# Optimization experiments

Measured on AMD Instinct MI355X. Metric: run time of the kernel, lower is better.

Reference implementation:

```python
import jax, jax.numpy as jnp
import numpy as np

N, D_IN, D_OUT = 4096, 1024, 1024

def setup_inputs() -> dict:
    key = jax.random.key(0)
    k1, k2, k3, k4 = jax.random.split(key, 4)
    x = jax.random.normal(k1, (N, D_IN), dtype=jnp.float32)
    # original uses torch.rand (uniform [0,1)) for params
    w_query = jax.random.uniform(k2, (D_IN, D_OUT), dtype=jnp.float32)
    w_key = jax.random.uniform(k3, (D_IN, D_OUT), dtype=jnp.float32)
    w_value = jax.random.uniform(k4, (D_IN, D_OUT), dtype=jnp.float32)
    return {"x": x, "w_query": w_query, "w_key": w_key, "w_value": w_value}

def reference(x, w_query, w_key, w_value):
    queries = x @ w_query          # [N, d_out]
    keys = x @ w_key               # [N, d_out]
    values = x @ w_value           # [N, d_out]
    scale = keys.shape[-1] ** 0.5
    scores = queries @ keys.T      # [N, N]
    attn = jax.nn.softmax(scores / scale, axis=-1)
    return attn @ values           # [N, d_out]
```

## Files before the change

kernel.cpp:

```cpp
#include <hip/hip_runtime.h>
#include <math.h>

#define NROWS 4096
#define DDIM  1024

typedef __attribute__((ext_vector_type(8))) short short8;
typedef __attribute__((ext_vector_type(4))) float f32x4;

__device__ __forceinline__ ushort f2bf(float v) {
  union { float f; uint32_t u; } c; c.f = v;
  uint32_t u = c.u;
  uint32_t lsb = (u >> 16) & 1u;
  u += 0x7fffu + lsb;
  return (ushort)(u >> 16);
}
__device__ __forceinline__ float bf2f(ushort h) {
  union { uint32_t u; float f; } c; c.u = ((uint32_t)h) << 16;
  return c.f;
}

__device__ __forceinline__ size_t pidx(int r, int c, int ldt) {
  return ((size_t)((r >> 4) * ldt + (c >> 5))) * 512 +
         ((c >> 3) & 3) * 128 + (r & 15) * 8 + (c & 7);
}

__global__ __launch_bounds__(256) void prep(const float* __restrict__ x,
                                            const float* __restrict__ wq,
                                            const float* __restrict__ wk,
                                            const float* __restrict__ wv,
                                            ushort* Xh, ushort* Xl,
                                            ushort* Wqh, ushort* Wql,
                                            ushort* Wkh, ushort* Wkl, ushort* Wvh) {
  __shared__ float tl[32][33];
  const int b = blockIdx.x, t = threadIdx.x;
  if (b < 1024) {
    const float4* src = (const float4*)x;
#pragma unroll
    for (int r = 0; r < 4; ++r) {
      int i = b * 1024 + r * 256 + t;
      int row = i >> 8;
      int c = (i & 255) << 2;
      float4 v = src[i];
      ushort4 h, l;
      h.x = f2bf(v.x); l.x = f2bf(v.x - bf2f(h.x));
      h.y = f2bf(v.y); l.y = f2bf(v.y - bf2f(h.y));
      h.z = f2bf(v.z); l.z = f2bf(v.z - bf2f(h.z));
      h.w = f2bf(v.w); l.w = f2bf(v.w - bf2f(h.w));
      size_t o = pidx(row, c, DDIM / 32);
      *(ushort4*)(Xh + o) = h;
      *(ushort4*)(Xl + o) = l;
    }
  } else {
    const int z = (b - 1024) >> 10;
    const int tile = (b - 1024) & 1023;
    const float* src = z == 0 ? wq : (z == 1 ? wk : wv);
    ushort* dh = z == 0 ? Wqh : (z == 1 ? Wkh : Wvh);
    ushort* dl = z == 0 ? Wql : (z == 1 ? Wkl : nullptr);
    const int r0 = (tile >> 5) * 32;
    const int c0 = (tile & 31) * 32;
    const int tx = t & 31, ty = t >> 5;
    for (int i = ty; i < 32; i += 8)
      tl[i][tx] = src[(size_t)(r0 + i) * DDIM + c0 + tx];
    __syncthreads();
    for (int i = ty; i < 32; i += 8) {
      float v = tl[tx][i];
      ushort h = f2bf(v);
      size_t o = pidx(c0 + i, r0 + tx, DDIM / 32);
      dh[o] = h;
      if (dl) dl[o] = f2bf(v - bf2f(h));
    }
  }
}

template <bool SPLIT, int KT>
__device__ __forceinline__ void direct_gemm(const ushort* __restrict__ Ah,
                                            const ushort* __restrict__ Al,
                                            const ushort* __restrict__ Bh,
                                            const ushort* __restrict__ Bl,
                                            int m0, int n0, f32x4 (*acc)[4]) {
  const int t = threadIdx.x;
  const int wv = t >> 6, ln = t & 63;
  const int arb = (wv >> 1) * 64, crb = (wv & 1) * 64;
  const int ra = (m0 + arb) >> 4;
  const int rb = (n0 + crb) >> 4;
  const size_t ts = (size_t)KT * 512;

  size_t baseA[4], baseB[4];
#pragma unroll
  for (int i = 0; i < 4; ++i) baseA[i] = (size_t)(ra + i) * ts + ln * 8;
#pragma unroll
  for (int j = 0; j < 4; ++j) baseB[j] = (size_t)(rb + j) * ts + ln * 8;

#pragma unroll 2
  for (int s = 0; s < KT; ++s) {
    short8 ah[4], al[4];
#pragma unroll
    for (int i = 0; i < 4; ++i) {
      size_t o = baseA[i] + (size_t)s * 512;
      ah[i] = *(const short8*)(Ah + o);
      if constexpr (SPLIT) al[i] = *(const short8*)(Al + o);
    }
#pragma unroll
    for (int j = 0; j < 4; ++j) {
      size_t o = baseB[j] + (size_t)s * 512;
      short8 bh = *(const short8*)(Bh + o);
#pragma unroll
      for (int i = 0; i < 4; ++i)
        acc[i][j] = __builtin_amdgcn_mfma_f32_16x16x32_bf16(ah[i], bh, acc[i][j], 0, 0, 0);
      if constexpr (SPLIT) {
        short8 bl = *(const short8*)(Bl + o);
#pragma unroll
        for (int i = 0; i < 4; ++i) {
          acc[i][j] = __builtin_amdgcn_mfma_f32_16x16x32_bf16(ah[i], bl, acc[i][j], 0, 0, 0);
          acc[i][j] = __builtin_amdgcn_mfma_f32_16x16x32_bf16(al[i], bh, acc[i][j], 0, 0, 0);
        }
      }
    }
  }
}

__global__ __launch_bounds__(256) void gemm_qkv(const ushort* __restrict__ Xh,
                                                const ushort* __restrict__ Xl,
                                                const ushort* __restrict__ Wqh, const ushort* __restrict__ Wql,
                                                const ushort* __restrict__ Wkh, const ushort* __restrict__ Wkl,
                                                const ushort* __restrict__ Wvh,
                                                ushort* Qh, ushort* Ql, ushort* Kh, ushort* Kl, ushort* Vt) {
  const int which = blockIdx.x % 3;
  const int g = blockIdx.x / 3;
  const int by = blockIdx.y;
  const int t = threadIdx.x;
  const int wv = t >> 6, ln = t & 63;
  const int quad = ln >> 4, l16 = ln & 15;

  f32x4 acc[4][4];
#pragma unroll
  for (int i = 0; i < 4; ++i)
#pragma unroll
    for (int j = 0; j < 4; ++j) acc[i][j] = (f32x4){0.f, 0.f, 0.f, 0.f};

  if (which == 2) {
    const int m0 = g * 128;
    const int n0 = by * 128;
    direct_gemm<false, DDIM / 32>(Wvh, nullptr, Xh, nullptr, m0, n0, acc);
#pragma unroll
    for (int i = 0; i < 4; ++i)
#pragma unroll
      for (int j = 0; j < 4; ++j) {
        int kv = n0 + (wv & 1) * 64 + j * 16 + l16;
        int d = m0 + (wv >> 1) * 64 + i * 16 + quad * 4;
#pragma unroll
        for (int r2 = 0; r2 < 4; ++r2)
          Vt[pidx(d + r2, kv, NROWS / 32)] = f2bf(acc[i][j][r2]);
      }
  } else {
    const int n0 = g * 128;
    const int m0 = by * 128;
    const ushort* Bh = which ? Wkh : Wqh;
    const ushort* Bl = which ? Wkl : Wql;
    direct_gemm<true, DDIM / 32>(Xh, Xl, Bh, Bl, m0, n0, acc);
    const float scale = which ? 1.0f : 0.03125f;
    ushort* H = which ? Kh : Qh;
    ushort* L = which ? Kl : Ql;
#pragma unroll
    for (int i = 0; i < 4; ++i)
#pragma unroll
      for (int j = 0; j < 4; ++j) {
        int col = n0 + (wv & 1) * 64 + j * 16 + l16;
        int rw = m0 + (wv >> 1) * 64 + i * 16 + quad * 4;
#pragma unroll
        for (int r2 = 0; r2 < 4; ++r2) {
          float v = acc[i][j][r2] * scale;
          ushort h = f2bf(v);
          size_t o = pidx(rw + r2, col, DDIM / 32);
          H[o] = h;
          L[o] = f2bf(v - bf2f(h));
        }
      }
  }
}

__global__ __launch_bounds__(256) void gemm_s(const ushort* __restrict__ Qh, const ushort* __restrict__ Ql,
                                              const ushort* __restrict__ Kh, const ushort* __restrict__ Kl,
                                              float* __restrict__ S) {
  const int n0 = blockIdx.x * 128, m0 = blockIdx.y * 128;
  const int t = threadIdx.x;
  const int wv = t >> 6, ln = t & 63;
  const int quad = ln >> 4, l16 = ln & 15;

  f32x4 acc[4][4];
#pragma unroll
  for (int i = 0; i < 4; ++i)
#pragma unroll
    for (int j = 0; j < 4; ++j) acc[i][j] = (f32x4){0.f, 0.f, 0.f, 0.f};

  direct_gemm<true, DDIM / 32>(Qh, Ql, Kh, Kl, m0, n0, acc);

#pragma unroll
  for (int i = 0; i < 4; ++i)
#pragma unroll
    for (int j = 0; j < 4; ++j) {
      int col = n0 + (wv & 1) * 64 + j * 16 + l16;
      int rw = m0 + (wv >> 1) * 64 + i * 16 + quad * 4;
#pragma unroll
      for (int r2 = 0; r2 < 4; ++r2)
        S[(size_t)(rw + r2) * NROWS + col] = acc[i][j][r2];
    }
}

__global__ __launch_bounds__(256) void softmax_pack(const float* __restrict__ S,
                                                    ushort* __restrict__ P) {
  const int row = blockIdx.x, t = threadIdx.x;
  const float* Sr = S + (size_t)row * NROWS;
  const float4* S4 = (const float4*)Sr;
  float4 v[4];
  float mx = -3.4e38f;
#pragma unroll
  for (int c = 0; c < 4; ++c) {
    v[c] = S4[c * 256 + t];
    mx = fmaxf(mx, fmaxf(fmaxf(v[c].x, v[c].y), fmaxf(v[c].z, v[c].w)));
  }
  __shared__ float red[4];
  for (int o = 32; o >= 1; o >>= 1) mx = fmaxf(mx, __shfl_xor(mx, o));
  int wv = t >> 6, ln = t & 63;
  if (ln == 0) red[wv] = mx;
  __syncthreads();
  mx = fmaxf(fmaxf(red[0], red[1]), fmaxf(red[2], red[3]));
  float s = 0.f;
#pragma unroll
  for (int c = 0; c < 4; ++c) {
    v[c].x = __expf(v[c].x - mx);
    v[c].y = __expf(v[c].y - mx);
    v[c].z = __expf(v[c].z - mx);
    v[c].w = __expf(v[c].w - mx);
    s += v[c].x + v[c].y + v[c].z + v[c].w;
  }
  for (int o = 32; o >= 1; o >>= 1) s += __shfl_xor(s, o);
  __syncthreads();
  if (ln == 0) red[wv] = s;
  __syncthreads();
  s = red[0] + red[1] + red[2] + red[3];
  float inv = 1.f / s;
#pragma unroll
  for (int c = 0; c < 4; ++c) {
    ushort4 h;
    h.x = f2bf(v[c].x * inv);
    h.y = f2bf(v[c].y * inv);
    h.z = f2bf(v[c].z * inv);
    h.w = f2bf(v[c].w * inv);
    int c0 = 1024 * c + 4 * t;
    *(ushort4*)(P + pidx(row, c0, NROWS / 32)) = h;
  }
}

__global__ __launch_bounds__(256) void gemm_pv(const ushort* __restrict__ P,
                                               const ushort* __restrict__ Vt,
                                               float* __restrict__ Out) {
  const int n0 = blockIdx.x * 128, m0 = blockIdx.y * 128;
  const int t = threadIdx.x;
  const int wv = t >> 6, ln = t & 63;
  const int quad = ln >> 4, l16 = ln & 15;

  f32x4 acc[4][4];
#pragma unroll
  for (int i = 0; i < 4; ++i)
#pragma unroll
    for (int j = 0; j < 4; ++j) acc[i][j] = (f32x4){0.f, 0.f, 0.f, 0.f};

  direct_gemm<false, NROWS / 32>(P, nullptr, Vt, nullptr, m0, n0, acc);

#pragma unroll
  for (int i = 0; i < 4; ++i)
#pragma unroll
    for (int j = 0; j < 4; ++j) {
      int col = n0 + (wv & 1) * 64 + j * 16 + l16;
      int rw = m0 + (wv >> 1) * 64 + i * 16 + quad * 4;
#pragma unroll
      for (int r2 = 0; r2 < 4; ++r2)
        Out[(size_t)(rw + r2) * DDIM + col] = acc[i][j][r2];
    }
}

extern "C" void kernel_launch(void* const* d_in, const int* in_sizes, int n_in,
                              void* d_out, int out_size, void* d_ws, size_t ws_size,
                              hipStream_t stream) {
  const float* x  = (const float*)d_in[0];
  const float* wq = (const float*)d_in[1];
  const float* wk = (const float*)d_in[2];
  const float* wv = (const float*)d_in[3];
  char* ws = (char*)d_ws;
  const size_t MB = 1u << 20;

  ushort* Vt  = (ushort*)(ws + 0);
  ushort* Qh  = (ushort*)(ws + 8 * MB);
  ushort* Ql  = (ushort*)(ws + 16 * MB);
  ushort* Kh  = (ushort*)(ws + 24 * MB);
  ushort* Kl  = (ushort*)(ws + 32 * MB);
  ushort* Pp  = (ushort*)(ws + 8 * MB);
  ushort* Xh  = (ushort*)(ws + 40 * MB);
  ushort* Xl  = (ushort*)(ws + 48 * MB);
  ushort* Wqh = (ushort*)(ws + 56 * MB);
  ushort* Wql = (ushort*)(ws + 58 * MB);
  ushort* Wkh = (ushort*)(ws + 60 * MB);
  ushort* Wkl = (ushort*)(ws + 62 * MB);
  ushort* Wvh = (ushort*)(ws + 64 * MB);
  float*  S   = (float*)(ws + 40 * MB);
  float*  Out = (float*)d_out;

  prep<<<4096, 256, 0, stream>>>(x, wq, wk, wv, Xh, Xl, Wqh, Wql, Wkh, Wkl, Wvh);
  gemm_qkv<<<dim3(24, 32), 256, 0, stream>>>(Xh, Xl, Wqh, Wql, Wkh, Wkl, Wvh,
                                             Qh, Ql, Kh, Kl, Vt);
  gemm_s<<<dim3(32, 32), 256, 0, stream>>>(Qh, Ql, Kh, Kl, S);
  softmax_pack<<<NROWS, 256, 0, stream>>>(S, Pp);
  gemm_pv<<<dim3(8, 32), 256, 0, stream>>>(Pp, Vt, Out);
}
```

Measured before the change: 345.7 us.

## Double-buffer register loads in direct GEMM and remap blocks for XCD locality

The inner GEMM loop is rewritten to prefetch the next K-step's A/B fragments into a second register set while MFMAs consume the current set, with s_setprio raised around the MFMA bursts. Offsets switch to 32-bit arithmetic. Both GEMM kernels remap block IDs so that blocks landing on the same XCD share row/column bands, improving L2 reuse. The cost is doubled fragment registers, which may raise VGPR pressure and lower occupancy.

```diff
diff --git a/kernel.cpp b/kernel.cpp
--- a/kernel.cpp
+++ b/kernel.cpp
@@ -83,40 +83,62 @@
   const int arb = (wv >> 1) * 64, crb = (wv & 1) * 64;
   const int ra = (m0 + arb) >> 4;
   const int rb = (n0 + crb) >> 4;
-  const size_t ts = (size_t)KT * 512;
-
-  size_t baseA[4], baseB[4];
-#pragma unroll
-  for (int i = 0; i < 4; ++i) baseA[i] = (size_t)(ra + i) * ts + ln * 8;
-#pragma unroll
-  for (int j = 0; j < 4; ++j) baseB[j] = (size_t)(rb + j) * ts + ln * 8;
-
-#pragma unroll 2
-  for (int s = 0; s < KT; ++s) {
-    short8 ah[4], al[4];
-#pragma unroll
-    for (int i = 0; i < 4; ++i) {
-      size_t o = baseA[i] + (size_t)s * 512;
-      ah[i] = *(const short8*)(Ah + o);
-      if constexpr (SPLIT) al[i] = *(const short8*)(Al + o);
-    }
-#pragma unroll
-    for (int j = 0; j < 4; ++j) {
-      size_t o = baseB[j] + (size_t)s * 512;
-      short8 bh = *(const short8*)(Bh + o);
-#pragma unroll
-      for (int i = 0; i < 4; ++i)
-        acc[i][j] = __builtin_amdgcn_mfma_f32_16x16x32_bf16(ah[i], bh, acc[i][j], 0, 0, 0);
-      if constexpr (SPLIT) {
-        short8 bl = *(const short8*)(Bl + o);
-#pragma unroll
-        for (int i = 0; i < 4; ++i) {
-          acc[i][j] = __builtin_amdgcn_mfma_f32_16x16x32_bf16(ah[i], bl, acc[i][j], 0, 0, 0);
-          acc[i][j] = __builtin_amdgcn_mfma_f32_16x16x32_bf16(al[i], bh, acc[i][j], 0, 0, 0);
-        }
-      }
-    }
-  }
+  const uint ts = (uint)KT * 512u;
+
+  uint oA[4], oB[4];
+#pragma unroll
+  for (int i = 0; i < 4; ++i) oA[i] = (uint)(ra + i) * ts + (uint)ln * 8u;
+#pragma unroll
+  for (int j = 0; j < 4; ++j) oB[j] = (uint)(rb + j) * ts + (uint)ln * 8u;
+
+  short8 ah0[4], al0[4], bh0[4], bl0[4];
+  short8 ah1[4], al1[4], bh1[4], bl1[4];
+
+#define DG_LOAD(sidx, AH, AL, BH, BL)                                        \
+  {                                                                          \
+    uint so_ = (uint)(sidx)*512u;                                            \
+    _Pragma("unroll") for (int i_ = 0; i_ < 4; ++i_) {                       \
+      AH[i_] = *(const short8*)(Ah + oA[i_] + so_);                          \
+      if constexpr (SPLIT) AL[i_] = *(const short8*)(Al + oA[i_] + so_);     \
+    }                                                                        \
+    _Pragma("unroll") for (int j_ = 0; j_ < 4; ++j_) {                       \
+      BH[j_] = *(const short8*)(Bh + oB[j_] + so_);                          \
+      if constexpr (SPLIT) BL[j_] = *(const short8*)(Bl + oB[j_] + so_);     \
+    }                                                                        \
+  }
+
+#define DG_MFMA(AH, AL, BH, BL)                                              \
+  {                                                                          \
+    __builtin_amdgcn_s_setprio(1);                                           \
+    _Pragma("unroll") for (int j_ = 0; j_ < 4; ++j_) {                       \
+      _Pragma("unroll") for (int i_ = 0; i_ < 4; ++i_) {                     \
+        acc[i_][j_] = __builtin_amdgcn_mfma_f32_16x16x32_bf16(               \
+            AH[i_], BH[j_], acc[i_][j_], 0, 0, 0);                           \
+        if constexpr (SPLIT) {                                               \
+          acc[i_][j_] = __builtin_amdgcn_mfma_f32_16x16x32_bf16(             \
+              AH[i_], BL[j_], acc[i_][j_], 0, 0, 0);                         \
+          acc[i_][j_] = __builtin_amdgcn_mfma_f32_16x16x32_bf16(             \
+              AL[i_], BH[j_], acc[i_][j_], 0, 0, 0);                         \
+        }                                                                    \
+      }                                                                      \
+    }                                                                        \
+    __builtin_amdgcn_s_setprio(0);                                           \
+  }
+
+  DG_LOAD(0, ah0, al0, bh0, bl0);
+#pragma unroll 1
+  for (int s = 0; s < KT - 2; s += 2) {
+    DG_LOAD(s + 1, ah1, al1, bh1, bl1);
+    DG_MFMA(ah0, al0, bh0, bl0);
+    DG_LOAD(s + 2, ah0, al0, bh0, bl0);
+    DG_MFMA(ah1, al1, bh1, bl1);
+  }
+  DG_LOAD(KT - 1, ah1, al1, bh1, bl1);
+  DG_MFMA(ah0, al0, bh0, bl0);
+  DG_MFMA(ah1, al1, bh1, bl1);
+
+#undef DG_LOAD
+#undef DG_MFMA
 }
 
 __global__ __launch_bounds__(256) void gemm_qkv(const ushort* __restrict__ Xh,
@@ -125,9 +147,11 @@
                                                 const ushort* __restrict__ Wkh, const ushort* __restrict__ Wkl,
                                                 const ushort* __restrict__ Wvh,
                                                 ushort* Qh, ushort* Ql, ushort* Kh, ushort* Kl, ushort* Vt) {
-  const int which = blockIdx.x % 3;
-  const int g = blockIdx.x / 3;
-  const int by = blockIdx.y;
+  const int id = blockIdx.y * 24 + blockIdx.x;
+  const int wg = (id & 7) * 96 + (id >> 3);
+  const int bx = wg % 24, by = wg / 24;
+  const int which = bx % 3;
+  const int g = bx / 3;
   const int t = threadIdx.x;
   const int wv = t >> 6, ln = t & 63;
   const int quad = ln >> 4, l16 = ln & 15;
@@ -182,7 +206,12 @@
 __global__ __launch_bounds__(256) void gemm_s(const ushort* __restrict__ Qh, const ushort* __restrict__ Ql,
                                               const ushort* __restrict__ Kh, const ushort* __restrict__ Kl,
                                               float* __restrict__ S) {
-  const int n0 = blockIdx.x * 128, m0 = blockIdx.y * 128;
+  const int bid = blockIdx.y * 32 + blockIdx.x;
+  const int xcd = bid & 7, local = bid >> 3;
+  const int band = xcd >> 1, half = xcd & 1;
+  const int row_l = local & 7, col_l = local >> 3;
+  const int m0 = (band * 8 + row_l) * 128;
+  const int n0 = (half * 16 + col_l) * 128;
   const int t = threadIdx.x;
   const int wv = t >> 6, ln = t & 63;
   const int quad = ln >> 4, l16 = ln & 15;
```

Measured after the change: 317.2 us. 1.09x faster.
